# Optimization experiments

Hardware: AMD Instinct MI355X
Metric: run time of the kernel (lower is better)

The kernel has to match this reference:

```python
import jax, jax.numpy as jnp
import numpy as np

GROUP_SIZE = 128  # K-rows sharing one dequant scale


def _dequant(B, s):
    """Unpack int4 (uint4b8: value = nibble - 8) from packed int32 and apply group scales.
    B: [K//8, N] int32, 8 nibbles per word along K (nibble i -> k = 8*row + i).
    s: [K//GROUP_SIZE, N] float scales.
    Returns W: [K, N] float.
    """
    Kp, N = B.shape
    K = Kp * 8
    shifts = (jnp.arange(8, dtype=jnp.int32) * 4)
    # [Kp, 8, N] nibbles -> [K, N]
    nib = (B[:, None, :] >> shifts[None, :, None]) & 0xF
    w = nib.reshape(K, N).astype(s.dtype) - 8.0
    # per-group scaling: groups of GROUP_SIZE consecutive K rows
    w = (w.reshape(K // GROUP_SIZE, GROUP_SIZE, N) * s[:, None, :]).reshape(K, N)
    return w


def setup_inputs() -> dict:
    key = jax.random.key(0)
    k1, k2, k3 = jax.random.split(key, 3)
    M, K, N = 64, 8192, 8192
    x = jax.random.normal(k1, (M, K), dtype=jnp.float32)
    B = jax.random.randint(k2, (K // 8, N), 0, 2147483647, dtype=jnp.int32)
    s = jax.random.uniform(k3, (K // GROUP_SIZE, N), dtype=jnp.float32) * 0.02
    return {"x": x, "B": B, "s": s}


def reference(x, B, s):
    # machete_mm: fused int4 dequant + GEMM; here expressed as dequant then matmul
    w = _dequant(B, s)          # [K, N]
    out = x @ w                 # [M, N]
    return out
```

## Files before the change

kernel.cpp:

```cpp
#include <hip/hip_runtime.h>

typedef _Float16 half2v __attribute__((ext_vector_type(2)));
typedef _Float16 half8  __attribute__((ext_vector_type(8)));
typedef float    floatx4 __attribute__((ext_vector_type(4)));

#define M_DIM 64
#define K_DIM 8192
#define N_DIM 8192
#define NT 64
#define KSB 8
#define STAGES 8

__global__ __launch_bounds__(256) void permute_x_kernel(
        const float* __restrict__ x, _Float16* __restrict__ xp) {
    const int t  = blockIdx.x * 256 + threadIdx.x;
    const int c  = t & 15;
    const int q  = (t >> 4) & 3;
    const int mt = (t >> 6) & 3;
    const int kb = t >> 8;
    const int m  = mt * 16 + c;
    const int k0 = kb * 32 + q * 8;
    const float* src = x + (size_t)m * K_DIM + k0;
    float4 a = *(const float4*)(src);
    float4 b = *(const float4*)(src + 4);
    union { _Float16 h[8]; float4 f; } u;
    u.h[0] = (_Float16)a.x; u.h[1] = (_Float16)b.x;
    u.h[2] = (_Float16)a.y; u.h[3] = (_Float16)b.y;
    u.h[4] = (_Float16)a.z; u.h[5] = (_Float16)b.z;
    u.h[6] = (_Float16)a.w; u.h[7] = (_Float16)b.w;
    *(float4*)(xp + (size_t)t * 8) = u.f;
}

__device__ __forceinline__ void dma16(const void* g, void* l) {
    __builtin_amdgcn_global_load_lds(
        (const __attribute__((address_space(1))) unsigned int*)(uintptr_t)g,
        (__attribute__((address_space(3))) unsigned int*)(uintptr_t)l,
        16, 0, 0);
}

__device__ __forceinline__ half2v dq_pair(unsigned int bits, half2v sub, half2v sc) {
    union { unsigned int u; half2v h; } cv;
    cv.u = bits;
    return (cv.h - sub) * sc;
}

__global__ __launch_bounds__(256, 3) void machete_mm_kernel(
        const _Float16* __restrict__ xp,
        const unsigned int* __restrict__ Bq,
        const float* __restrict__ s,
        float* __restrict__ partial) {
    union SM {
        char stage[2][20480];
        float red[4][32][65];
    };
    __shared__ SM sm;

    const int tid  = threadIdx.x;
    const int w    = tid >> 6;
    const int lane = tid & 63;
    const int c    = lane & 15;
    const int q    = lane >> 4;
    const int n0   = blockIdx.x * NT;
    const int kb0  = blockIdx.y * (K_DIM / KSB);
    const int ncol = n0 + 4 * c;

    const char* a_base = (const char*)xp + (size_t)(kb0 >> 5) * 4096;
    const char* b_base = (const char*)Bq + ((size_t)(kb0 >> 3) * N_DIM + n0) * 4;
    const size_t b_lane = (size_t)(lane >> 4) * ((size_t)N_DIM * 4) + (size_t)(lane & 15) * 16;
    const int    a_lane = lane * 16;

    floatx4 acc[4][4];
    #pragma unroll
    for (int i = 0; i < 4; ++i)
        #pragma unroll
        for (int j = 0; j < 4; ++j) acc[i][j] = (floatx4)0.0f;

    const half2v c1032 = { (_Float16)1032.0f, (_Float16)1032.0f };

    auto stage_dma = [&](int si, int p) {
        const char* as = a_base + (size_t)si * 16384;
        #pragma unroll
        for (int call = 0; call < 4; ++call) {
            const int idx = call * 4 + w;
            dma16(as + idx * 1024 + a_lane, &sm.stage[p][idx * 1024]);
        }
        const char* bs = b_base + (size_t)(si * 16 + w * 4) * ((size_t)N_DIM * 4) + b_lane;
        dma16(bs, &sm.stage[p][16384 + w * 1024]);
    };

    stage_dma(0, 0);
    __syncthreads();

    for (int st = 0; st < STAGES; ++st) {
        const int p = st & 1;

        const float4 s4 = *(const float4*)(s + (size_t)((kb0 >> 7) + st) * N_DIM + ncol);

        if (st + 1 < STAGES) stage_dma(st + 1, p ^ 1);

        half2v s2[4];
        s2[0] = (half2v){ (_Float16)s4.x, (_Float16)s4.x };
        s2[1] = (half2v){ (_Float16)s4.y, (_Float16)s4.y };
        s2[2] = (half2v){ (_Float16)s4.z, (_Float16)s4.z };
        s2[3] = (half2v){ (_Float16)s4.w, (_Float16)s4.w };

        const char* ab = &sm.stage[p][w * 4096];
        half8 afr[4];
        #pragma unroll
        for (int mt = 0; mt < 4; ++mt)
            afr[mt] = *(const half8*)(ab + mt * 1024 + a_lane);
        union { uint4 v; unsigned int a[4]; } bv;
        bv.v = *(const uint4*)(&sm.stage[p][16384 + w * 1024 + q * 256 + c * 16]);

        #pragma unroll
        for (int t = 0; t < 4; ++t) {
            const unsigned int wd = bv.a[t];
            const half2v sc = s2[t];
            union { half2v h2[4]; half8 h8; } b8;
            b8.h2[0] = dq_pair(( wd        & 0x000F000Fu) | 0x64006400u, c1032, sc);
            b8.h2[1] = dq_pair(((wd >> 4)  & 0x000F000Fu) | 0x64006400u, c1032, sc);
            b8.h2[2] = dq_pair(((wd >> 8)  & 0x000F000Fu) | 0x64006400u, c1032, sc);
            b8.h2[3] = dq_pair(((wd >> 12) & 0x000F000Fu) | 0x64006400u, c1032, sc);
            #pragma unroll
            for (int mt = 0; mt < 4; ++mt)
                acc[mt][t] = __builtin_amdgcn_mfma_f32_16x16x32_f16(
                    afr[mt], b8.h8, acc[mt][t], 0, 0, 0);
        }

        __syncthreads();
    }

    float* ptile = partial + ((size_t)blockIdx.y * M_DIM) * N_DIM + n0;
    #pragma unroll
    for (int r = 0; r < 2; ++r) {
        if (r) __syncthreads();
        #pragma unroll
        for (int h = 0; h < 2; ++h) {
            const int mt = 2 * r + h;
            #pragma unroll
            for (int t = 0; t < 4; ++t)
                #pragma unroll
                for (int rr = 0; rr < 4; ++rr)
                    sm.red[w][h * 16 + q * 4 + rr][4 * c + t] = acc[mt][t][rr];
        }
        __syncthreads();
        #pragma unroll
        for (int i = 0; i < 8; ++i) {
            const int idx = i * 256 + tid;
            const int mr  = idx >> 6;
            const int nl  = idx & 63;
            const float v = sm.red[0][mr][nl] + sm.red[1][mr][nl]
                          + sm.red[2][mr][nl] + sm.red[3][mr][nl];
            ptile[(size_t)(r * 32 + mr) * N_DIM + nl] = v;
        }
    }
}

__global__ __launch_bounds__(256) void reduce_kernel(
        const float* __restrict__ partial, float* __restrict__ out) {
    const size_t i = ((size_t)blockIdx.x * 256 + threadIdx.x) * 4;
    const size_t S = (size_t)M_DIM * N_DIM;
    float4 v = *(const float4*)(partial + i);
    #pragma unroll
    for (int bk = 1; bk < KSB; ++bk) {
        const float4 u = *(const float4*)(partial + bk * S + i);
        v.x += u.x; v.y += u.y; v.z += u.z; v.w += u.w;
    }
    *(float4*)(out + i) = v;
}

extern "C" void kernel_launch(void* const* d_in, const int* in_sizes, int n_in,
                              void* d_out, int out_size, void* d_ws, size_t ws_size,
                              hipStream_t stream) {
    const float*        x  = (const float*)d_in[0];
    const unsigned int* Bq = (const unsigned int*)d_in[1];
    const float*        sc = (const float*)d_in[2];
    float* out     = (float*)d_out;
    _Float16* xp   = (_Float16*)d_ws;
    float* partial = (float*)((char*)d_ws + (1 << 20));

    permute_x_kernel<<<dim3(M_DIM * K_DIM / 8 / 256), 256, 0, stream>>>(x, xp);
    machete_mm_kernel<<<dim3(N_DIM / NT, KSB), 256, 0, stream>>>(xp, Bq, sc, partial);
    reduce_kernel<<<dim3(M_DIM * N_DIM / (256 * 4)), 256, 0, stream>>>(partial, out);
}
```

Before: 98.89 us.

## Restructure int4 GEMM: 1024-thread blocks, register-direct B loads, fp16 partials

Each block now covers 512 columns with 16 waves and a split-K of 16. Every wave owns its own 32-column slice and loads packed int4 weights straight from global memory into registers, prefetching one stage ahead. Only the shared activation tile is staged through LDS, and the cross-wave LDS reduction is removed because waves no longer split K inside a block. Partial sums are stored as fp16 to halve the partial-buffer traffic in the reduce kernel, at the cost of precision in the split-K accumulation.

```diff
diff --git a/kernel.cpp b/kernel.cpp
--- a/kernel.cpp
+++ b/kernel.cpp
@@ -7,9 +7,8 @@
 #define M_DIM 64
 #define K_DIM 8192
 #define N_DIM 8192
-#define NT 64
-#define KSB 8
-#define STAGES 8
+#define NT 512
+#define KSB 16
 
 __global__ __launch_bounds__(256) void permute_x_kernel(
         const float* __restrict__ x, _Float16* __restrict__ xp) {
@@ -44,129 +43,118 @@
     return (cv.h - sub) * sc;
 }
 
-__global__ __launch_bounds__(256, 3) void machete_mm_kernel(
+__global__ __launch_bounds__(1024, 4) void machete_mm_kernel(
         const _Float16* __restrict__ xp,
         const unsigned int* __restrict__ Bq,
         const float* __restrict__ s,
-        float* __restrict__ partial) {
-    union SM {
-        char stage[2][20480];
-        float red[4][32][65];
-    };
-    __shared__ SM sm;
+        _Float16* __restrict__ partial) {
+    __shared__ char astage[2][16384];
 
     const int tid  = threadIdx.x;
     const int w    = tid >> 6;
     const int lane = tid & 63;
     const int c    = lane & 15;
     const int q    = lane >> 4;
-    const int n0   = blockIdx.x * NT;
-    const int kb0  = blockIdx.y * (K_DIM / KSB);
-    const int ncol = n0 + 4 * c;
+    const int ns   = blockIdx.x;
+    const int kb   = blockIdx.y;
+    const int wc   = ns * NT + w * 32;
 
-    const char* a_base = (const char*)xp + (size_t)(kb0 >> 5) * 4096;
-    const char* b_base = (const char*)Bq + ((size_t)(kb0 >> 3) * N_DIM + n0) * 4;
-    const size_t b_lane = (size_t)(lane >> 4) * ((size_t)N_DIM * 4) + (size_t)(lane & 15) * 16;
-    const int    a_lane = lane * 16;
-
-    floatx4 acc[4][4];
+    half2v s2[4][2];
     #pragma unroll
-    for (int i = 0; i < 4; ++i)
-        #pragma unroll
-        for (int j = 0; j < 4; ++j) acc[i][j] = (floatx4)0.0f;
-
+    for (int g = 0; g < 4; ++g) {
+        const float f0 = s[(size_t)(kb * 4 + g) * N_DIM + wc + c];
+        const float f1 = s[(size_t)(kb * 4 + g) * N_DIM + wc + 16 + c];
+        s2[g][0] = (half2v){ (_Float16)f0, (_Float16)f0 };
+        s2[g][1] = (half2v){ (_Float16)f1, (_Float16)f1 };
+    }
     const half2v c1032 = { (_Float16)1032.0f, (_Float16)1032.0f };
 
-    auto stage_dma = [&](int si, int p) {
-        const char* as = a_base + (size_t)si * 16384;
-        #pragma unroll
-        for (int call = 0; call < 4; ++call) {
-            const int idx = call * 4 + w;
-            dma16(as + idx * 1024 + a_lane, &sm.stage[p][idx * 1024]);
-        }
-        const char* bs = b_base + (size_t)(si * 16 + w * 4) * ((size_t)N_DIM * 4) + b_lane;
-        dma16(bs, &sm.stage[p][16384 + w * 1024]);
+    const char* a_base = (const char*)xp + (size_t)kb * 65536;
+    const unsigned int* b_base = Bq + (size_t)(kb * 64) * N_DIM + wc + c;
+
+    auto bload = [&](int st, int d, int t) {
+        return b_base[(size_t)(st * 16 + d * 4 + q) * N_DIM + 16 * t];
+    };
+    auto stage_dma = [&](int st, int p) {
+        dma16(a_base + (size_t)st * 16384 + w * 1024 + lane * 16,
+              &astage[p][w * 1024]);
     };
 
+    floatx4 acc[4][2];
+    #pragma unroll
+    for (int i = 0; i < 4; ++i) { acc[i][0] = (floatx4)0.0f; acc[i][1] = (floatx4)0.0f; }
+
+    unsigned int bcur[2][4], bnxt[2][4];
+    #pragma unroll
+    for (int d = 0; d < 4; ++d) { bcur[0][d] = bload(0, d, 0); bcur[1][d] = bload(0, d, 1); }
     stage_dma(0, 0);
     __syncthreads();
 
-    for (int st = 0; st < STAGES; ++st) {
+    #pragma unroll
+    for (int st = 0; st < 4; ++st) {
         const int p = st & 1;
-
-        const float4 s4 = *(const float4*)(s + (size_t)((kb0 >> 7) + st) * N_DIM + ncol);
-
-        if (st + 1 < STAGES) stage_dma(st + 1, p ^ 1);
-
-        half2v s2[4];
-        s2[0] = (half2v){ (_Float16)s4.x, (_Float16)s4.x };
-        s2[1] = (half2v){ (_Float16)s4.y, (_Float16)s4.y };
-        s2[2] = (half2v){ (_Float16)s4.z, (_Float16)s4.z };
-        s2[3] = (half2v){ (_Float16)s4.w, (_Float16)s4.w };
-
-        const char* ab = &sm.stage[p][w * 4096];
-        half8 afr[4];
-        #pragma unroll
-        for (int mt = 0; mt < 4; ++mt)
-            afr[mt] = *(const half8*)(ab + mt * 1024 + a_lane);
-        union { uint4 v; unsigned int a[4]; } bv;
-        bv.v = *(const uint4*)(&sm.stage[p][16384 + w * 1024 + q * 256 + c * 16]);
+        if (st < 3) {
+            #pragma unroll
+            for (int d = 0; d < 4; ++d) {
+                bnxt[0][d] = bload(st + 1, d, 0);
+                bnxt[1][d] = bload(st + 1, d, 1);
+            }
+            stage_dma(st + 1, p ^ 1);
+        }
 
         #pragma unroll
-        for (int t = 0; t < 4; ++t) {
-            const unsigned int wd = bv.a[t];
-            const half2v sc = s2[t];
-            union { half2v h2[4]; half8 h8; } b8;
-            b8.h2[0] = dq_pair(( wd        & 0x000F000Fu) | 0x64006400u, c1032, sc);
-            b8.h2[1] = dq_pair(((wd >> 4)  & 0x000F000Fu) | 0x64006400u, c1032, sc);
-            b8.h2[2] = dq_pair(((wd >> 8)  & 0x000F000Fu) | 0x64006400u, c1032, sc);
-            b8.h2[3] = dq_pair(((wd >> 12) & 0x000F000Fu) | 0x64006400u, c1032, sc);
+        for (int d = 0; d < 4; ++d) {
+            half8 afr[4];
             #pragma unroll
             for (int mt = 0; mt < 4; ++mt)
-                acc[mt][t] = __builtin_amdgcn_mfma_f32_16x16x32_f16(
-                    afr[mt], b8.h8, acc[mt][t], 0, 0, 0);
-        }
-
-        __syncthreads();
-    }
-
-    float* ptile = partial + ((size_t)blockIdx.y * M_DIM) * N_DIM + n0;
-    #pragma unroll
-    for (int r = 0; r < 2; ++r) {
-        if (r) __syncthreads();
-        #pragma unroll
-        for (int h = 0; h < 2; ++h) {
-            const int mt = 2 * r + h;
+                afr[mt] = *(const half8*)(&astage[p][(d * 4 + mt) * 1024 + lane * 16]);
             #pragma unroll
-            for (int t = 0; t < 4; ++t)
+            for (int t = 0; t < 2; ++t) {
+                const unsigned int wd = bcur[t][d];
+                const half2v sc = s2[st][t];
+                union { half2v h2[4]; half8 h8; } b8;
+                b8.h2[0] = dq_pair(( wd        & 0x000F000Fu) | 0x64006400u, c1032, sc);
+                b8.h2[1] = dq_pair(((wd >> 4)  & 0x000F000Fu) | 0x64006400u, c1032, sc);
+                b8.h2[2] = dq_pair(((wd >> 8)  & 0x000F000Fu) | 0x64006400u, c1032, sc);
+                b8.h2[3] = dq_pair(((wd >> 12) & 0x000F000Fu) | 0x64006400u, c1032, sc);
                 #pragma unroll
-                for (int rr = 0; rr < 4; ++rr)
-                    sm.red[w][h * 16 + q * 4 + rr][4 * c + t] = acc[mt][t][rr];
+                for (int mt = 0; mt < 4; ++mt)
+                    acc[mt][t] = __builtin_amdgcn_mfma_f32_16x16x32_f16(
+                        afr[mt], b8.h8, acc[mt][t], 0, 0, 0);
+            }
         }
         __syncthreads();
         #pragma unroll
-        for (int i = 0; i < 8; ++i) {
-            const int idx = i * 256 + tid;
-            const int mr  = idx >> 6;
-            const int nl  = idx & 63;
-            const float v = sm.red[0][mr][nl] + sm.red[1][mr][nl]
-                          + sm.red[2][mr][nl] + sm.red[3][mr][nl];
-            ptile[(size_t)(r * 32 + mr) * N_DIM + nl] = v;
-        }
+        for (int d = 0; d < 4; ++d) { bcur[0][d] = bnxt[0][d]; bcur[1][d] = bnxt[1][d]; }
     }
+
+    _Float16* pt = partial + (size_t)(kb * M_DIM) * N_DIM;
+    #pragma unroll
+    for (int mt = 0; mt < 4; ++mt)
+        #pragma unroll
+        for (int t = 0; t < 2; ++t)
+            #pragma unroll
+            for (int r = 0; r < 4; ++r) {
+                const int m = mt * 16 + q * 4 + r;
+                pt[(size_t)m * N_DIM + wc + 16 * t + c] = (_Float16)acc[mt][t][r];
+            }
 }
 
 __global__ __launch_bounds__(256) void reduce_kernel(
-        const float* __restrict__ partial, float* __restrict__ out) {
-    const size_t i = ((size_t)blockIdx.x * 256 + threadIdx.x) * 4;
+        const _Float16* __restrict__ partial, float* __restrict__ out) {
+    const size_t i = ((size_t)blockIdx.x * 256 + threadIdx.x) * 8;
     const size_t S = (size_t)M_DIM * N_DIM;
-    float4 v = *(const float4*)(partial + i);
+    float a[8] = {0, 0, 0, 0, 0, 0, 0, 0};
     #pragma unroll
-    for (int bk = 1; bk < KSB; ++bk) {
-        const float4 u = *(const float4*)(partial + bk * S + i);
-        v.x += u.x; v.y += u.y; v.z += u.z; v.w += u.w;
+    for (int bk = 0; bk < KSB; ++bk) {
+        const half8 hv = *(const half8*)(partial + bk * S + i);
+        #pragma unroll
+        for (int j = 0; j < 8; ++j) a[j] += (float)hv[j];
     }
-    *(float4*)(out + i) = v;
+    float4 v0 = { a[0], a[1], a[2], a[3] };
+    float4 v1 = { a[4], a[5], a[6], a[7] };
+    *(float4*)(out + i)     = v0;
+    *(float4*)(out + i + 4) = v1;
 }
 
 extern "C" void kernel_launch(void* const* d_in, const int* in_sizes, int n_in,
@@ -175,11 +163,11 @@
     const float*        x  = (const float*)d_in[0];
     const unsigned int* Bq = (const unsigned int*)d_in[1];
     const float*        sc = (const float*)d_in[2];
-    float* out     = (float*)d_out;
-    _Float16* xp   = (_Float16*)d_ws;
-    float* partial = (float*)((char*)d_ws + (1 << 20));
+    float* out        = (float*)d_out;
+    _Float16* xp      = (_Float16*)d_ws;
+    _Float16* partial = (_Float16*)((char*)d_ws + (1 << 20));
 
     permute_x_kernel<<<dim3(M_DIM * K_DIM / 8 / 256), 256, 0, stream>>>(x, xp);
-    machete_mm_kernel<<<dim3(N_DIM / NT, KSB), 256, 0, stream>>>(xp, Bq, sc, partial);
-    reduce_kernel<<<dim3(M_DIM * N_DIM / (256 * 4)), 256, 0, stream>>>(partial, out);
+    machete_mm_kernel<<<dim3(N_DIM / NT, KSB), 1024, 0, stream>>>(xp, Bq, sc, partial);
+    reduce_kernel<<<dim3(M_DIM * N_DIM / (256 * 8)), 256, 0, stream>>>(partial, out);
 }
```

New measurement: 96.05 us. 1.03x faster.
